# Kernel optimization log

Hardware: AMD Instinct MI355X
Metric: run time of the kernel (lower is better)

Reference implementation:

```python
import jax, jax.numpy as jnp
import numpy as np
from jax import lax
import math

C = 32            # num_channles
L_IN = 1024       # input signal length (forced by feature_size=520 constraint)
B = 1024          # batch


def _unfold(x, k, s):
    # x: (B, C, L) -> (B, C, n, k), torch Tensor.unfold(dim=2, size=k, step=s)
    n = (x.shape[-1] - k) // s + 1
    idx = np.arange(n)[:, None] * s + np.arange(k)[None, :]
    return x[..., idx]


def _always(x, w, b):
    # Conv1DAlwaysLayer: beta - sum_k (1 - window)*w, then relu, then leaky_relu(0.02)
    win = _unfold(x, 8, 2)                                  # (B,C,n,8)
    r = b[None, :, None] - jnp.einsum('bcnk,ck->bcn', 1.0 - win, w)
    return jax.nn.leaky_relu(jax.nn.relu(r), 0.02)


def _eventually(x, w, b):
    # Conv1DEventuallyLayer: relu(1 - (beta - sum_k window*w)), then leaky_relu(0.02)
    win = _unfold(x, 8, 2)
    r = 1.0 - (b[None, :, None] - jnp.einsum('bcnk,ck->bcn', win, w))
    return jax.nn.leaky_relu(jax.nn.relu(r), 0.02)


def _bn(x, g, b):
    # BatchNorm1d in training mode: batch statistics over (B, L), biased var
    m = x.mean(axis=(0, 2), keepdims=True)
    v = ((x - m) ** 2).mean(axis=(0, 2), keepdims=True)
    return (x - m) * jax.lax.rsqrt(v + 1e-5) * g[None, :, None] + b[None, :, None]


def _avgpool(x, k, s):
    return _unfold(x, k, s).mean(axis=-1)


def _maxpool(x, k, s):
    return _unfold(x, k, s).max(axis=-1)


def _laplace_filters(la_a, la_b):
    # LaplacePredicate filter bank: (C, 1, 16)
    A, ep, tal, f = 0.08, 0.03, 0.1, 50.0
    w = 2.0 * math.pi * f
    q = 1.0 - ep ** 2
    t = jnp.linspace(0.0, 1.0, 16, dtype=jnp.float32)       # kernel_size -> 16
    p = t[None, :] - (la_b / la_a)                           # (C,16)
    y = A * jnp.exp(-ep / math.sqrt(q) * (w * (p - tal))) * (-jnp.sin(w * (p - tal)))
    return y.reshape(C, 1, 16)


def setup_inputs() -> dict:
    key = jax.random.key(0)
    ks = jax.random.split(key, 32)
    rn = lambda k, shp: jax.random.normal(k, shp, dtype=jnp.float32)
    inp = {
        'x': rn(ks[0], (B, 1, L_IN)),
        # LaplacePredicate params
        'la_a': jnp.linspace(1.0, 10.0, C, dtype=jnp.float32).reshape(C, 1),
        'la_b': jnp.linspace(0.0, 10.0, C, dtype=jnp.float32).reshape(C, 1),
        'la_bias': rn(ks[1], (C,)),
        # BatchNorm after predicate
        'bn1_g': rn(ks[2], (C,)) * 0.1 + 1.0,
        'bn1_b': rn(ks[3], (C,)) * 0.1,
        # conv1d branch: Always -> Eventually -> MaxPool -> BN -> Eventually
        'a1_w': rn(ks[4], (C, 8)), 'a1_b': rn(ks[5], (C,)),
        'e1_w': rn(ks[6], (C, 8)), 'e1_b': rn(ks[7], (C,)),
        'bn2_g': rn(ks[8], (C,)) * 0.1 + 1.0, 'bn2_b': rn(ks[9], (C,)) * 0.1,
        'e2_w': rn(ks[10], (C, 8)), 'e2_b': rn(ks[11], (C,)),
        # conv1dFG branch: Eventually -> Always -> MaxPool -> BN -> Eventually
        'f1_w': rn(ks[12], (C, 8)), 'f1_b': rn(ks[13], (C,)),
        'fa_w': rn(ks[14], (C, 8)), 'fa_b': rn(ks[15], (C,)),
        'bn3_g': rn(ks[16], (C,)) * 0.1 + 1.0, 'bn3_b': rn(ks[17], (C,)) * 0.1,
        'f2_w': rn(ks[18], (C, 8)), 'f2_b': rn(ks[19], (C,)),
        # fc: 768 -> 1024 -> 512 -> 128 -> 10 (W stored (in,out))
        'w1': rn(ks[20], (768, 1024)) * (768 ** -0.5), 'b1': rn(ks[21], (1024,)) * 0.01,
        'w2': rn(ks[22], (1024, 512)) * (1024 ** -0.5), 'b2': rn(ks[23], (512,)) * 0.01,
        'w3': rn(ks[24], (512, 128)) * (512 ** -0.5), 'b3': rn(ks[25], (128,)) * 0.01,
        'w4': rn(ks[26], (128, 10)) * (128 ** -0.5), 'b4': rn(ks[27], (10,)) * 0.01,
    }
    return inp


def _forward(x, la_a, la_b, la_bias, bn1_g, bn1_b,
             a1_w, a1_b, e1_w, e1_b, bn2_g, bn2_b, e2_w, e2_b,
             f1_w, f1_b, fa_w, fa_b, bn3_g, bn3_b, f2_w, f2_b,
             w1, b1, w2, b2, w3, b3, w4, b4):
    # predicate_pos: LaplacePredicate -> BN -> AvgPool(3,2)
    filt = _laplace_filters(la_a, la_b)                      # (32,1,16)
    h = lax.conv_general_dilated(x, filt, window_strides=(1,),
                                 padding=[(16, 16)])         # (B,32,1041)
    h = h + la_bias[None, :, None]
    h = _bn(h, bn1_g, bn1_b)
    h = _avgpool(h, 3, 2)                                    # (B,32,520)
    # NOTE: fuseautoencoder/norm path in the source is dead code (result unused)
    # conv1d branch
    x1 = _always(h, a1_w, a1_b)                              # (B,32,257)
    x1 = _eventually(x1, e1_w, e1_b)                         # (B,32,125)
    x1 = _maxpool(x1, 4, 4)                                  # (B,32,31)
    x1 = _bn(x1, bn2_g, bn2_b)
    x1 = _eventually(x1, e2_w, e2_b)                         # (B,32,12)
    # conv1dFG branch
    x2 = _eventually(h, f1_w, f1_b)
    x2 = _always(x2, fa_w, fa_b)
    x2 = _maxpool(x2, 4, 4)
    x2 = _bn(x2, bn3_g, bn3_b)
    x2 = _eventually(x2, f2_w, f2_b)                         # (B,32,12)
    z = jnp.concatenate([x1, x2], axis=1).reshape(x.shape[0], -1)  # (B,768)
    z = jax.nn.relu(z @ w1 + b1)
    z = jax.nn.relu(z @ w2 + b2)    # Dropout -> identity (eval)
    z = jax.nn.relu(z @ w3 + b3)
    z = jax.nn.relu(z @ w4 + b4)
    return z                                                 # (B,10)


def reference(x, la_a, la_b, la_bias, bn1_g, bn1_b,
              a1_w, a1_b, e1_w, e1_b, bn2_g, bn2_b, e2_w, e2_b,
              f1_w, f1_b, fa_w, fa_b, bn3_g, bn3_b, f2_w, f2_b,
              w1, b1, w2, b2, w3, b3, w4, b4):
    return _forward(x, la_a, la_b, la_bias, bn1_g, bn1_b,
                    a1_w, a1_b, e1_w, e1_b, bn2_g, bn2_b, e2_w, e2_b,
                    f1_w, f1_b, fa_w, fa_b, bn3_g, bn3_b, f2_w, f2_b,
                    w1, b1, w2, b2, w3, b3, w4, b4)
```

## Files before the change

### kernel.cpp

```cpp
#include <hip/hip_runtime.h>
#include <math.h>


#define L_MP 31

using s8v = __attribute__((ext_vector_type(8))) short;
using f4v = __attribute__((ext_vector_type(4))) float;

__device__ __forceinline__ ushort f2bf(float f) {
    unsigned u = __float_as_uint(f);
    u += 0x7fffu + ((u >> 16) & 1u);
    return (ushort)(u >> 16);
}
__device__ __forceinline__ float bf2f(ushort u) {
    return __uint_as_float(((unsigned)u) << 16);
}

__global__ __launch_bounds__(256) void xstats_kernel(
    const float* __restrict__ x, double* __restrict__ xp)
{
    __shared__ __align__(16) float xr[1040];
    __shared__ float wred[4][17];
    int b = blockIdx.x, tid = threadIdx.x;
    for (int i = tid; i < 1024; i += 256) xr[i] = x[b * 1024 + i];
    if (tid < 16) xr[1024 + tid] = 0.f;
    __syncthreads();
    float acc[17];
#pragma unroll
    for (int d = 0; d < 17; ++d) acc[d] = 0.f;
    for (int p = tid; p < 1024; p += 256) {
        float v = xr[p];
        acc[16] += v;
#pragma unroll
        for (int d = 0; d < 16; ++d)
            acc[d] += v * xr[p + d];
    }
#pragma unroll
    for (int off = 32; off >= 1; off >>= 1)
#pragma unroll
        for (int d = 0; d < 17; ++d)
            acc[d] += __shfl_down(acc[d], off);
    int wave = tid >> 6, lane = tid & 63;
    if (lane == 0)
        for (int d = 0; d < 17; ++d) wred[wave][d] = acc[d];
    __syncthreads();
    if (tid < 17) {
        double tot = (double)wred[0][tid] + (double)wred[1][tid]
                   + (double)wred[2][tid] + (double)wred[3][tid];
        xp[tid * 1024 + b] = tot;
    }
}

__global__ __launch_bounds__(256) void reduce_x_kernel(
    const double* __restrict__ xp, double* __restrict__ stats)
{
    __shared__ double wr[4];
    int d = blockIdx.x, t = threadIdx.x;
    const double* r = xp + (size_t)d * 1024;
    double a = r[t] + r[t + 256] + r[t + 512] + r[t + 768];
#pragma unroll
    for (int off = 32; off >= 1; off >>= 1) a += __shfl_down(a, off);
    int wv = t >> 6, lane = t & 63;
    if (lane == 0) wr[wv] = a;
    __syncthreads();
    if (t == 0) stats[d] = wr[0] + wr[1] + wr[2] + wr[3];
}

__global__ __launch_bounds__(512) void prep_kernel(
    const double* __restrict__ stats,
    const float* __restrict__ la_a, const float* __restrict__ la_b,
    const float* __restrict__ bn1_g, const float* __restrict__ bn1_b,
    float* __restrict__ g18_out, float* __restrict__ a1d1_out)
{
    __shared__ float fs[32][16];
    int tid = threadIdx.x;
    if (tid < 512) {
        int c = tid >> 4, k = tid & 15;
        const double A = 0.08, ep = 0.03, tal = 0.1;
        const double w = 2.0 * 3.14159265358979323846 * 50.0;
        const double q = 1.0 - ep * ep;
        double t = (double)k / 15.0;
        double p = t - (double)la_b[c] / (double)la_a[c];
        double arg = w * (p - tal);
        double y = A * exp(-ep / sqrt(q) * arg) * (-sin(arg));
        fs[c][k] = (float)y;
    }
    __syncthreads();
    if (tid < 32) {
        int c = tid;
        for (int i = 0; i < 18; ++i) {
            float g = 0.f;
            for (int k = i - 2; k <= i; ++k)
                if (k >= 0 && k < 16) g += fs[c][k];
            g18_out[c * 18 + i] = g;
        }
        double Sf = 0.0;
        for (int k = 0; k < 16; ++k) Sf += (double)fs[c][k];
        double E2 = 0.0;
        for (int k = 0; k < 16; ++k)
            for (int k2 = 0; k2 < 16; ++k2)
                E2 += (double)fs[c][k] * (double)fs[c][k2]
                    * stats[k > k2 ? k - k2 : k2 - k];
        const double N = 1024.0 * 1041.0;
        double Sx = stats[16];
        double mc  = Sx * Sf / N;
        double var = E2 / N - mc * mc;
        double invstd = 1.0 / sqrt(var + 1e-5);
        float alpha = bn1_g[c] * (float)invstd;
        a1d1_out[c]      = alpha / 3.0f;
        a1d1_out[32 + c] = bn1_b[c] - (float)mc * alpha;
    }
}

__global__ __launch_bounds__(512) void branches_kernel(
    const float* __restrict__ x,
    const float* __restrict__ g18g, const float* __restrict__ a1d1,
    const float* __restrict__ a1w_g, const float* __restrict__ a1b_g,
    const float* __restrict__ e1w_g, const float* __restrict__ e1b_g,
    const float* __restrict__ f1w_g, const float* __restrict__ f1b_g,
    const float* __restrict__ faw_g, const float* __restrict__ fab_g,
    float* __restrict__ p1, float* __restrict__ p2,
    float* __restrict__ bp)
{
    __shared__ float xs[1140];
    __shared__ float g18s[32][18];
    __shared__ float wts[4][32][8];
    __shared__ float htail[32][6];

    int b = blockIdx.x, t = threadIdx.x;
    int wv = t >> 6, lane = t & 63;

    for (int i = t; i < 1072; i += 512) {
        float v = 0.f;
        if (i >= 16 && i < 1040) v = x[(size_t)b * 1024 + (i - 16)];
        xs[i + (i >> 4)] = v;
    }
    if (t < 288) ((float2*)&g18s[0][0])[t] = ((const float2*)g18g)[t];
    if (t < 256) {
        wts[0][0][t] = a1w_g[t];
        wts[1][0][t] = e1w_g[t];
        wts[2][0][t] = f1w_g[t];
        wts[3][0][t] = faw_g[t];
    }
    __syncthreads();

    if (t < 192) {
        int c = t / 6, e = t - 6 * (t / 6);
        float s = 0.f;
#pragma unroll
        for (int i = 0; i < 18; ++i) {
            int li = 1024 + 2 * e + i;
            s += g18s[c][i] * xs[li + (li >> 4)];
        }
        htail[c][e] = s * a1d1[c] + a1d1[32 + c];
    }
    __syncthreads();

    for (int cc = 0; cc < 4; ++cc) {
        int c = (cc << 3) + wv;
        float alpha = a1d1[c], delta = a1d1[32 + c];

        float hv[8];
        {
            float g[18];
#pragma unroll
            for (int i = 0; i < 18; ++i) g[i] = g18s[c][i];
            int base = 17 * lane;
            float xw[32];
#pragma unroll
            for (int q = 0; q < 16; ++q) xw[q] = xs[base + q];
#pragma unroll
            for (int q = 0; q < 16; ++q) xw[16 + q] = xs[base + 17 + q];
#pragma unroll
            for (int jj = 0; jj < 8; ++jj) {
                float s = 0.f;
#pragma unroll
                for (int i = 0; i < 18; ++i) s += g[i] * xw[2 * jj + i];
                hv[jj] = s * alpha + delta;
            }
        }

        float x1v[4], x2v[4];
        {
            float hx[14];
#pragma unroll
            for (int q = 0; q < 8; ++q) hx[q] = hv[q];
#pragma unroll
            for (int q = 0; q < 6; ++q) {
                float u = __shfl_down(hv[q], 1);
                float tl = htail[c][q];
                hx[8 + q] = (lane == 63) ? tl : u;
            }
            float wa[8], wf[8];
            float A1 = a1b_g[c], F1 = 1.f - f1b_g[c];
#pragma unroll
            for (int k = 0; k < 8; ++k) {
                wa[k] = wts[0][c][k];
                wf[k] = wts[2][c][k];
                A1 -= wa[k];
            }
#pragma unroll
            for (int nn = 0; nn < 4; ++nn) {
                float s1 = A1, s2 = F1;
#pragma unroll
                for (int k = 0; k < 8; ++k) {
                    float h = hx[2 * nn + k];
                    s1 += h * wa[k];
                    s2 += h * wf[k];
                }
                x1v[nn] = s1 > 0.f ? s1 : 0.f;
                x2v[nn] = s2 > 0.f ? s2 : 0.f;
            }
        }

        float y1v[2], y2v[2];
        {
            float xx1[10], xx2[10];
#pragma unroll
            for (int q = 0; q < 4; ++q) { xx1[q] = x1v[q]; xx2[q] = x2v[q]; }
#pragma unroll
            for (int q = 0; q < 4; ++q) {
                xx1[4 + q] = __shfl_down(x1v[q], 1);
                xx2[4 + q] = __shfl_down(x2v[q], 1);
            }
#pragma unroll
            for (int q = 0; q < 2; ++q) {
                xx1[8 + q] = __shfl_down(x1v[q], 2);
                xx2[8 + q] = __shfl_down(x2v[q], 2);
            }
            float we[8], wfa[8];
            float E1 = 1.f - e1b_g[c], FA = fab_g[c];
#pragma unroll
            for (int k = 0; k < 8; ++k) {
                we[k]  = wts[1][c][k];
                wfa[k] = wts[3][c][k];
                FA -= wfa[k];
            }
#pragma unroll
            for (int mm = 0; mm < 2; ++mm) {
                float s1 = E1, s2 = FA;
#pragma unroll
                for (int k = 0; k < 8; ++k) {
                    s1 += xx1[2 * mm + k] * we[k];
                    s2 += xx2[2 * mm + k] * wfa[k];
                }
                y1v[mm] = s1 > 0.f ? s1 : 0.f;
                y2v[mm] = s2 > 0.f ? s2 : 0.f;
            }
        }

        {
            int sa = 2 * lane, sb = 2 * lane + 1;
            float a0 = __shfl(y1v[0], sa), a1q = __shfl(y1v[1], sa);
            float a2 = __shfl(y1v[0], sb), a3 = __shfl(y1v[1], sb);
            float b0 = __shfl(y2v[0], sa), b1q = __shfl(y2v[1], sa);
            float b2 = __shfl(y2v[0], sb), b3 = __shfl(y2v[1], sb);
            float v1 = fmaxf(fmaxf(a0, a1q), fmaxf(a2, a3));
            float v2 = fmaxf(fmaxf(b0, b1q), fmaxf(b2, b3));
            bool valid = lane < L_MP;
            if (valid) {
                int bc = b * 32 + c;
                p1[(size_t)bc * L_MP + lane] = v1;
                p2[(size_t)bc * L_MP + lane] = v2;
            }
            float s1 = valid ? v1 : 0.f, q1 = valid ? v1 * v1 : 0.f;
            float s2 = valid ? v2 : 0.f, q2 = valid ? v2 * v2 : 0.f;
#pragma unroll
            for (int off = 16; off >= 1; off >>= 1) {
                s1 += __shfl_down(s1, off);
                q1 += __shfl_down(q1, off);
                s2 += __shfl_down(s2, off);
                q2 += __shfl_down(q2, off);
            }
            if (lane == 0) {
                bp[(size_t)(c)      * 1024 + b] = s1;
                bp[(size_t)(32 + c) * 1024 + b] = q1;
                bp[(size_t)(64 + c) * 1024 + b] = s2;
                bp[(size_t)(96 + c) * 1024 + b] = q2;
            }
        }
    }
}

__global__ __launch_bounds__(256) void reduce_bn_kernel(
    const float* __restrict__ bp, double* __restrict__ bn_d)
{
    __shared__ double wr[4];
    int r = blockIdx.x, t = threadIdx.x;
    const float* p = bp + (size_t)r * 1024;
    double a = (double)p[t] + (double)p[t + 256]
             + (double)p[t + 512] + (double)p[t + 768];
#pragma unroll
    for (int off = 32; off >= 1; off >>= 1) a += __shfl_down(a, off);
    int wv = t >> 6, lane = t & 63;
    if (lane == 0) wr[wv] = a;
    __syncthreads();
    if (t == 0) bn_d[r] = wr[0] + wr[1] + wr[2] + wr[3];
}

__global__ void bn23_finalize_kernel(
    const double* __restrict__ bn_d,
    const float* __restrict__ bn2_g, const float* __restrict__ bn2_b,
    const float* __restrict__ bn3_g, const float* __restrict__ bn3_b,
    float* __restrict__ ad23)
{
    int t = threadIdx.x;
    if (t < 64) {
        int br = t >> 5, c = t & 31;
        double sum = bn_d[br * 64 + c], sq = bn_d[br * 64 + 32 + c];
        const double N = 1024.0 * 31.0;
        double mean = sum / N;
        double var = sq / N - mean * mean;
        float g  = br ? bn3_g[c] : bn2_g[c];
        float be = br ? bn3_b[c] : bn2_b[c];
        float alpha = g * (float)(1.0 / sqrt(var + 1e-5));
        ad23[br * 64 + c]      = alpha;
        ad23[br * 64 + 32 + c] = be - (float)mean * alpha;
    }
}

__global__ __launch_bounds__(256) void final_ev_kernel(
    const float* __restrict__ p1, const float* __restrict__ p2,
    const float* __restrict__ e2w_g, const float* __restrict__ e2b_g,
    const float* __restrict__ f2w_g, const float* __restrict__ f2b_g,
    const float* __restrict__ ad23, ushort* __restrict__ z0)
{
    __shared__ float pr[2][32][31];
    __shared__ float w2s[2][32][8];
    __shared__ float al[2][32], de[2][32], eb[2][32];
    int b = blockIdx.x, tid = threadIdx.x;
    for (int i = tid; i < 992; i += 256) {
        pr[0][0][i] = p1[b * 992 + i];
        pr[1][0][i] = p2[b * 992 + i];
    }
    if (tid < 256) {
        w2s[0][0][tid] = e2w_g[tid];
        w2s[1][0][tid] = f2w_g[tid];
    }
    if (tid < 32) {
        al[0][tid] = ad23[tid];      de[0][tid] = ad23[32 + tid];
        al[1][tid] = ad23[64 + tid]; de[1][tid] = ad23[96 + tid];
        eb[0][tid] = e2b_g[tid];     eb[1][tid] = f2b_g[tid];
    }
    __syncthreads();
    for (int u = tid; u < 768; u += 256) {
        int br = u / 384, rem = u - br * 384;
        int c = rem / 12, tt = rem - c * 12;
        float a = al[br][c], d = de[br][c];
        float s = 1.f - eb[br][c];
#pragma unroll
        for (int k = 0; k < 8; ++k)
            s += (pr[br][c][2 * tt + k] * a + d) * w2s[br][c][k];
        z0[(size_t)b * 768 + u] = f2bf(s > 0.f ? s : 0.f);
    }
}

__global__ __launch_bounds__(256) void transpose_bf16_kernel(
    const float* __restrict__ W, ushort* __restrict__ Wt, int K, int N)
{
    __shared__ float tile[32][33];
    int n0 = blockIdx.x * 32, k0 = blockIdx.y * 32;
    int tx = threadIdx.x & 31, ty = threadIdx.x >> 5;
#pragma unroll
    for (int i = 0; i < 4; ++i)
        tile[ty + 8 * i][tx] = W[(size_t)(k0 + ty + 8 * i) * N + n0 + tx];
    __syncthreads();
#pragma unroll
    for (int i = 0; i < 4; ++i)
        Wt[(size_t)(n0 + ty + 8 * i) * K + k0 + tx] = f2bf(tile[tx][ty + 8 * i]);
}

__global__ __launch_bounds__(256) void gemm_mfma_kernel(
    const ushort* __restrict__ A, const ushort* __restrict__ Bt,
    const float* __restrict__ bias, ushort* __restrict__ C,
    int N, int K)
{
    int w = blockIdx.x * 4 + (threadIdx.x >> 6);
    int lane = threadIdx.x & 63;
    int ntiles = N >> 4;
    int mt = w / ntiles, nt = w - mt * ntiles;
    int r = lane & 15, q = lane >> 4;
    const ushort* ap = A + (size_t)(mt * 16 + r) * K + q * 8;
    const ushort* bp = Bt + (size_t)(nt * 16 + r) * K + q * 8;
    f4v acc = {0.f, 0.f, 0.f, 0.f};
    int nk = K >> 5;
    s8v a0 = *(const s8v*)ap;
    s8v b0 = *(const s8v*)bp;
#pragma unroll 4
    for (int i = 0; i < nk; ++i) {
        int j = (i + 1 < nk) ? i + 1 : i;
        s8v a1 = *(const s8v*)(ap + (size_t)j * 32);
        s8v b1 = *(const s8v*)(bp + (size_t)j * 32);
        acc = __builtin_amdgcn_mfma_f32_16x16x32_bf16(a0, b0, acc, 0, 0, 0);
        a0 = a1; b0 = b1;
    }
    float bv = bias[nt * 16 + r];
    int row0 = mt * 16 + q * 4;
    int col = nt * 16 + r;
#pragma unroll
    for (int rr = 0; rr < 4; ++rr) {
        float v = acc[rr] + bv;
        v = v > 0.f ? v : 0.f;
        C[(size_t)(row0 + rr) * N + col] = f2bf(v);
    }
}

__global__ __launch_bounds__(256) void fc4_kernel(
    const ushort* __restrict__ z3, const float* __restrict__ w4,
    const float* __restrict__ b4, float* __restrict__ out)
{
    int g = blockIdx.x * 256 + threadIdx.x;
    if (g >= 1024 * 10) return;
    int m = g / 10, n = g - m * 10;
    float acc = b4[n];
#pragma unroll 8
    for (int k = 0; k < 128; ++k)
        acc += bf2f(z3[m * 128 + k]) * w4[k * 10 + n];
    out[g] = acc > 0.f ? acc : 0.f;
}

extern "C" void kernel_launch(void* const* d_in, const int* in_sizes, int n_in,
                              void* d_out, int out_size, void* d_ws, size_t ws_size,
                              hipStream_t stream)
{
    (void)in_sizes; (void)n_in; (void)out_size; (void)ws_size;
    const float* x      = (const float*)d_in[0];
    const float* la_a   = (const float*)d_in[1];
    const float* la_b   = (const float*)d_in[2];
    const float* bn1_g  = (const float*)d_in[4];
    const float* bn1_b  = (const float*)d_in[5];
    const float* a1_w   = (const float*)d_in[6];
    const float* a1_b   = (const float*)d_in[7];
    const float* e1_w   = (const float*)d_in[8];
    const float* e1_b   = (const float*)d_in[9];
    const float* bn2_g  = (const float*)d_in[10];
    const float* bn2_b  = (const float*)d_in[11];
    const float* e2_w   = (const float*)d_in[12];
    const float* e2_b   = (const float*)d_in[13];
    const float* f1_w   = (const float*)d_in[14];
    const float* f1_b   = (const float*)d_in[15];
    const float* fa_w   = (const float*)d_in[16];
    const float* fa_b   = (const float*)d_in[17];
    const float* bn3_g  = (const float*)d_in[18];
    const float* bn3_b  = (const float*)d_in[19];
    const float* f2_w   = (const float*)d_in[20];
    const float* f2_b   = (const float*)d_in[21];
    const float* w1     = (const float*)d_in[22];
    const float* b1     = (const float*)d_in[23];
    const float* w2     = (const float*)d_in[24];
    const float* b2     = (const float*)d_in[25];
    const float* w3     = (const float*)d_in[26];
    const float* b3     = (const float*)d_in[27];
    const float* w4     = (const float*)d_in[28];
    const float* b4     = (const float*)d_in[29];
    float* out = (float*)d_out;

    char* w = (char*)d_ws;
    double* stats_d = (double*)(w + 0);
    double* bn_d    = (double*)(w + 256);
    float* g18      = (float*)(w + 1536);
    float* a1d1     = (float*)(w + 3840);
    float* ad23     = (float*)(w + 4096);
    float* p1       = (float*)(w + 8192);
    float* p2       = (float*)(w + 4071424);
    ushort* z0bf    = (ushort*)(w + 8134656);
    ushort* z1bf    = (ushort*)(w + 9707520);
    ushort* z2bf    = (ushort*)(w + 11804672);
    ushort* z3bf    = (ushort*)(w + 12853248);
    ushort* wt1     = (ushort*)(w + 13115392);
    ushort* wt2     = (ushort*)(w + 14688256);
    ushort* wt3     = (ushort*)(w + 15736832);
    double* xp      = (double*)(w + 15867904);
    float*  bpart   = (float*)(w + 16007168);

    transpose_bf16_kernel<<<dim3(32, 24), 256, 0, stream>>>(w1, wt1, 768, 1024);
    transpose_bf16_kernel<<<dim3(16, 32), 256, 0, stream>>>(w2, wt2, 1024, 512);
    transpose_bf16_kernel<<<dim3(4, 16), 256, 0, stream>>>(w3, wt3, 512, 128);

    xstats_kernel<<<1024, 256, 0, stream>>>(x, xp);
    reduce_x_kernel<<<17, 256, 0, stream>>>(xp, stats_d);
    prep_kernel<<<1, 512, 0, stream>>>(stats_d, la_a, la_b, bn1_g, bn1_b, g18, a1d1);
    branches_kernel<<<1024, 512, 0, stream>>>(
        x, g18, a1d1, a1_w, a1_b, e1_w, e1_b, f1_w, f1_b, fa_w, fa_b,
        p1, p2, bpart);
    reduce_bn_kernel<<<128, 256, 0, stream>>>(bpart, bn_d);
    bn23_finalize_kernel<<<1, 64, 0, stream>>>(bn_d, bn2_g, bn2_b, bn3_g, bn3_b, ad23);
    final_ev_kernel<<<1024, 256, 0, stream>>>(p1, p2, e2_w, e2_b, f2_w, f2_b, ad23, z0bf);

    gemm_mfma_kernel<<<1024, 256, 0, stream>>>(z0bf, wt1, b1, z1bf, 1024, 768);
    gemm_mfma_kernel<<<512, 256, 0, stream>>>(z1bf, wt2, b2, z2bf, 512, 1024);
    gemm_mfma_kernel<<<128, 256, 0, stream>>>(z2bf, wt3, b3, z3bf, 128, 512);
    fc4_kernel<<<40, 256, 0, stream>>>(z3bf, w4, b4, out);
}
```

Before: 234.6 us.

## Merge small reduction kernels, split branches per channel half, batch weight transposes

```diff
diff --git a/kernel.cpp b/kernel.cpp
--- a/kernel.cpp
+++ b/kernel.cpp
@@ -51,30 +51,26 @@
     }
 }
 
-__global__ __launch_bounds__(256) void reduce_x_kernel(
-    const double* __restrict__ xp, double* __restrict__ stats)
-{
-    __shared__ double wr[4];
-    int d = blockIdx.x, t = threadIdx.x;
-    const double* r = xp + (size_t)d * 1024;
-    double a = r[t] + r[t + 256] + r[t + 512] + r[t + 768];
-#pragma unroll
-    for (int off = 32; off >= 1; off >>= 1) a += __shfl_down(a, off);
-    int wv = t >> 6, lane = t & 63;
-    if (lane == 0) wr[wv] = a;
-    __syncthreads();
-    if (t == 0) stats[d] = wr[0] + wr[1] + wr[2] + wr[3];
-}
-
 __global__ __launch_bounds__(512) void prep_kernel(
-    const double* __restrict__ stats,
+    const double* __restrict__ xp,
     const float* __restrict__ la_a, const float* __restrict__ la_b,
     const float* __restrict__ bn1_g, const float* __restrict__ bn1_b,
     float* __restrict__ g18_out, float* __restrict__ a1d1_out)
 {
+    __shared__ double stats[17];
     __shared__ float fs[32][16];
-    int tid = threadIdx.x;
-    if (tid < 512) {
+    int tid = threadIdx.x, wv = tid >> 6, lane = tid & 63;
+
+    for (int row = wv; row < 17; row += 8) {
+        const double* r = xp + (size_t)row * 1024;
+        double a = 0.0;
+        for (int i = lane; i < 1024; i += 64) a += r[i];
+#pragma unroll
+        for (int off = 32; off >= 1; off >>= 1) a += __shfl_down(a, off);
+        if (lane == 0) stats[row] = a;
+    }
+
+    {
         int c = tid >> 4, k = tid & 15;
         const double A = 0.08, ep = 0.03, tal = 0.1;
         const double w = 2.0 * 3.14159265358979323846 * 50.0;
@@ -112,65 +108,71 @@
     }
 }
 
-__global__ __launch_bounds__(512) void branches_kernel(
+__global__ __launch_bounds__(256) void branches_kernel(
     const float* __restrict__ x,
     const float* __restrict__ g18g, const float* __restrict__ a1d1,
     const float* __restrict__ a1w_g, const float* __restrict__ a1b_g,
     const float* __restrict__ e1w_g, const float* __restrict__ e1b_g,
     const float* __restrict__ f1w_g, const float* __restrict__ f1b_g,
     const float* __restrict__ faw_g, const float* __restrict__ fab_g,
-    float* __restrict__ p1, float* __restrict__ p2,
-    float* __restrict__ bp)
+    float* __restrict__ p1, float* __restrict__ p2)
 {
     __shared__ float xs[1140];
-    __shared__ float g18s[32][18];
-    __shared__ float wts[4][32][8];
-    __shared__ float htail[32][6];
-
-    int b = blockIdx.x, t = threadIdx.x;
+    __shared__ float g18s[16][18];
+    __shared__ float wts[4][16][8];
+    __shared__ float htail[16][6];
+
+    int blk = blockIdx.x;
+    int b = blk >> 1, hf = blk & 1;
+    int t = threadIdx.x;
     int wv = t >> 6, lane = t & 63;
 
-    for (int i = t; i < 1072; i += 512) {
+    for (int i = t; i < 1072; i += 256) {
         float v = 0.f;
         if (i >= 16 && i < 1040) v = x[(size_t)b * 1024 + (i - 16)];
         xs[i + (i >> 4)] = v;
     }
-    if (t < 288) ((float2*)&g18s[0][0])[t] = ((const float2*)g18g)[t];
-    if (t < 256) {
-        wts[0][0][t] = a1w_g[t];
-        wts[1][0][t] = e1w_g[t];
-        wts[2][0][t] = f1w_g[t];
-        wts[3][0][t] = faw_g[t];
-    }
-    __syncthreads();
-
-    if (t < 192) {
-        int c = t / 6, e = t - 6 * (t / 6);
+    if (t < 144) ((float2*)&g18s[0][0])[t] = ((const float2*)(g18g + hf * 288))[t];
+    if (t < 128) {
+        wts[0][0][t] = a1w_g[hf * 128 + t];
+        wts[1][0][t] = e1w_g[hf * 128 + t];
+        wts[2][0][t] = f1w_g[hf * 128 + t];
+        wts[3][0][t] = faw_g[hf * 128 + t];
+    }
+    __syncthreads();
+
+    if (t < 96) {
+        int cl = t / 6, e = t - 6 * (t / 6);
+        int cg = hf * 16 + cl;
         float s = 0.f;
 #pragma unroll
         for (int i = 0; i < 18; ++i) {
             int li = 1024 + 2 * e + i;
-            s += g18s[c][i] * xs[li + (li >> 4)];
-        }
-        htail[c][e] = s * a1d1[c] + a1d1[32 + c];
-    }
-    __syncthreads();
+            s += g18s[cl][i] * xs[li + (li >> 4)];
+        }
+        htail[cl][e] = s * a1d1[cg] + a1d1[32 + cg];
+    }
+    __syncthreads();
+
+    float xw[32];
+    {
+        int base = 17 * lane;
+#pragma unroll
+        for (int q = 0; q < 16; ++q) xw[q] = xs[base + q];
+#pragma unroll
+        for (int q = 0; q < 16; ++q) xw[16 + q] = xs[base + 17 + q];
+    }
 
     for (int cc = 0; cc < 4; ++cc) {
-        int c = (cc << 3) + wv;
-        float alpha = a1d1[c], delta = a1d1[32 + c];
+        int cl = wv * 4 + cc;
+        int cg = hf * 16 + cl;
+        float alpha = a1d1[cg], delta = a1d1[32 + cg];
 
         float hv[8];
         {
             float g[18];
 #pragma unroll
-            for (int i = 0; i < 18; ++i) g[i] = g18s[c][i];
-            int base = 17 * lane;
-            float xw[32];
-#pragma unroll
-            for (int q = 0; q < 16; ++q) xw[q] = xs[base + q];
-#pragma unroll
-            for (int q = 0; q < 16; ++q) xw[16 + q] = xs[base + 17 + q];
+            for (int i = 0; i < 18; ++i) g[i] = g18s[cl][i];
 #pragma unroll
             for (int jj = 0; jj < 8; ++jj) {
                 float s = 0.f;
@@ -188,15 +190,15 @@
 #pragma unroll
             for (int q = 0; q < 6; ++q) {
                 float u = __shfl_down(hv[q], 1);
-                float tl = htail[c][q];
+                float tl = htail[cl][q];
                 hx[8 + q] = (lane == 63) ? tl : u;
             }
             float wa[8], wf[8];
-            float A1 = a1b_g[c], F1 = 1.f - f1b_g[c];
+            float A1 = a1b_g[cg], F1 = 1.f - f1b_g[cg];
 #pragma unroll
             for (int k = 0; k < 8; ++k) {
-                wa[k] = wts[0][c][k];
-                wf[k] = wts[2][c][k];
+                wa[k] = wts[0][cl][k];
+                wf[k] = wts[2][cl][k];
                 A1 -= wa[k];
             }
 #pragma unroll
@@ -229,11 +231,11 @@
                 xx2[8 + q] = __shfl_down(x2v[q], 2);
             }
             float we[8], wfa[8];
-            float E1 = 1.f - e1b_g[c], FA = fab_g[c];
+            float E1 = 1.f - e1b_g[cg], FA = fab_g[cg];
 #pragma unroll
             for (int k = 0; k < 8; ++k) {
-                we[k]  = wts[1][c][k];
-                wfa[k] = wts[3][c][k];
+                we[k]  = wts[1][cl][k];
+                wfa[k] = wts[3][cl][k];
                 FA -= wfa[k];
             }
 #pragma unroll
@@ -250,63 +252,73 @@
         }
 
         {
-            int sa = 2 * lane, sb = 2 * lane + 1;
-            float a0 = __shfl(y1v[0], sa), a1q = __shfl(y1v[1], sa);
-            float a2 = __shfl(y1v[0], sb), a3 = __shfl(y1v[1], sb);
-            float b0 = __shfl(y2v[0], sa), b1q = __shfl(y2v[1], sa);
-            float b2 = __shfl(y2v[0], sb), b3 = __shfl(y2v[1], sb);
-            float v1 = fmaxf(fmaxf(a0, a1q), fmaxf(a2, a3));
-            float v2 = fmaxf(fmaxf(b0, b1q), fmaxf(b2, b3));
-            bool valid = lane < L_MP;
-            if (valid) {
-                int bc = b * 32 + c;
-                p1[(size_t)bc * L_MP + lane] = v1;
-                p2[(size_t)bc * L_MP + lane] = v2;
-            }
-            float s1 = valid ? v1 : 0.f, q1 = valid ? v1 * v1 : 0.f;
-            float s2 = valid ? v2 : 0.f, q2 = valid ? v2 * v2 : 0.f;
-#pragma unroll
-            for (int off = 16; off >= 1; off >>= 1) {
-                s1 += __shfl_down(s1, off);
-                q1 += __shfl_down(q1, off);
-                s2 += __shfl_down(s2, off);
-                q2 += __shfl_down(q2, off);
-            }
-            if (lane == 0) {
-                bp[(size_t)(c)      * 1024 + b] = s1;
-                bp[(size_t)(32 + c) * 1024 + b] = q1;
-                bp[(size_t)(64 + c) * 1024 + b] = s2;
-                bp[(size_t)(96 + c) * 1024 + b] = q2;
-            }
-        }
-    }
-}
-
-__global__ __launch_bounds__(256) void reduce_bn_kernel(
-    const float* __restrict__ bp, double* __restrict__ bn_d)
-{
-    __shared__ double wr[4];
-    int r = blockIdx.x, t = threadIdx.x;
-    const float* p = bp + (size_t)r * 1024;
-    double a = (double)p[t] + (double)p[t + 256]
-             + (double)p[t + 512] + (double)p[t + 768];
-#pragma unroll
-    for (int off = 32; off >= 1; off >>= 1) a += __shfl_down(a, off);
-    int wv = t >> 6, lane = t & 63;
-    if (lane == 0) wr[wv] = a;
-    __syncthreads();
-    if (t == 0) bn_d[r] = wr[0] + wr[1] + wr[2] + wr[3];
-}
-
-__global__ void bn23_finalize_kernel(
+            float m1 = fmaxf(y1v[0], y1v[1]);
+            float m2 = fmaxf(y2v[0], y2v[1]);
+            float n1 = __shfl_down(m1, 1);
+            float n2 = __shfl_down(m2, 1);
+            int tt = lane >> 1;
+            if (!(lane & 1) && tt < L_MP) {
+                int bc = b * 32 + cg;
+                p1[(size_t)bc * L_MP + tt] = fmaxf(m1, n1);
+                p2[(size_t)bc * L_MP + tt] = fmaxf(m2, n2);
+            }
+        }
+    }
+}
+
+__global__ __launch_bounds__(256) void pstats_kernel(
+    const float* __restrict__ p1, const float* __restrict__ p2,
+    double* __restrict__ bn_d)
+{
+    __shared__ double wr[4][2];
+    int bx = blockIdx.x, arr = bx >> 5, c = bx & 31;
+    const float* p = arr ? p2 : p1;
+    int t = threadIdx.x, wv = t >> 6, lane = t & 63;
+    double s = 0.0, q = 0.0;
+    for (int bb = t; bb < 1024; bb += 256) {
+        const float* r = p + ((size_t)bb * 32 + c) * L_MP;
+#pragma unroll
+        for (int j = 0; j < L_MP; ++j) {
+            double v = (double)r[j];
+            s += v; q += v * v;
+        }
+    }
+#pragma unroll
+    for (int off = 32; off >= 1; off >>= 1) {
+        s += __shfl_down(s, off);
+        q += __shfl_down(q, off);
+    }
+    if (lane == 0) { wr[wv][0] = s; wr[wv][1] = q; }
+    __syncthreads();
+    if (t == 0) {
+        bn_d[arr * 64 + c]      = wr[0][0] + wr[1][0] + wr[2][0] + wr[3][0];
+        bn_d[arr * 64 + 32 + c] = wr[0][1] + wr[1][1] + wr[2][1] + wr[3][1];
+    }
+}
+
+__global__ __launch_bounds__(256) void final_ev_kernel(
+    const float* __restrict__ p1, const float* __restrict__ p2,
+    const float* __restrict__ e2w_g, const float* __restrict__ e2b_g,
+    const float* __restrict__ f2w_g, const float* __restrict__ f2b_g,
     const double* __restrict__ bn_d,
     const float* __restrict__ bn2_g, const float* __restrict__ bn2_b,
     const float* __restrict__ bn3_g, const float* __restrict__ bn3_b,
-    float* __restrict__ ad23)
-{
-    int t = threadIdx.x;
-    if (t < 64) {
-        int br = t >> 5, c = t & 31;
+    ushort* __restrict__ z0)
+{
+    __shared__ float pr[2][32][31];
+    __shared__ float w2s[2][32][8];
+    __shared__ float al[2][32], de[2][32], eb[2][32];
+    int b = blockIdx.x, tid = threadIdx.x;
+    for (int i = tid; i < 992; i += 256) {
+        pr[0][0][i] = p1[b * 992 + i];
+        pr[1][0][i] = p2[b * 992 + i];
+    }
+    {
+        w2s[0][0][tid] = e2w_g[tid];
+        w2s[1][0][tid] = f2w_g[tid];
+    }
+    if (tid < 64) {
+        int br = tid >> 5, c = tid & 31;
         double sum = bn_d[br * 64 + c], sq = bn_d[br * 64 + 32 + c];
         const double N = 1024.0 * 31.0;
         double mean = sum / N;
@@ -314,33 +326,9 @@
         float g  = br ? bn3_g[c] : bn2_g[c];
         float be = br ? bn3_b[c] : bn2_b[c];
         float alpha = g * (float)(1.0 / sqrt(var + 1e-5));
-        ad23[br * 64 + c]      = alpha;
-        ad23[br * 64 + 32 + c] = be - (float)mean * alpha;
-    }
-}
-
-__global__ __launch_bounds__(256) void final_ev_kernel(
-    const float* __restrict__ p1, const float* __restrict__ p2,
-    const float* __restrict__ e2w_g, const float* __restrict__ e2b_g,
-    const float* __restrict__ f2w_g, const float* __restrict__ f2b_g,
-    const float* __restrict__ ad23, ushort* __restrict__ z0)
-{
-    __shared__ float pr[2][32][31];
-    __shared__ float w2s[2][32][8];
-    __shared__ float al[2][32], de[2][32], eb[2][32];
-    int b = blockIdx.x, tid = threadIdx.x;
-    for (int i = tid; i < 992; i += 256) {
-        pr[0][0][i] = p1[b * 992 + i];
-        pr[1][0][i] = p2[b * 992 + i];
-    }
-    if (tid < 256) {
-        w2s[0][0][tid] = e2w_g[tid];
-        w2s[1][0][tid] = f2w_g[tid];
-    }
-    if (tid < 32) {
-        al[0][tid] = ad23[tid];      de[0][tid] = ad23[32 + tid];
-        al[1][tid] = ad23[64 + tid]; de[1][tid] = ad23[96 + tid];
-        eb[0][tid] = e2b_g[tid];     eb[1][tid] = f2b_g[tid];
+        al[br][c] = alpha;
+        de[br][c] = be - (float)mean * alpha;
+        eb[br][c] = br ? f2b_g[c] : e2b_g[c];
     }
     __syncthreads();
     for (int u = tid; u < 768; u += 256) {
@@ -355,11 +343,18 @@
     }
 }
 
-__global__ __launch_bounds__(256) void transpose_bf16_kernel(
-    const float* __restrict__ W, ushort* __restrict__ Wt, int K, int N)
+__global__ __launch_bounds__(256) void transpose_all_kernel(
+    const float* __restrict__ w1, const float* __restrict__ w2,
+    const float* __restrict__ w3,
+    ushort* __restrict__ wt1, ushort* __restrict__ wt2, ushort* __restrict__ wt3)
 {
     __shared__ float tile[32][33];
-    int n0 = blockIdx.x * 32, k0 = blockIdx.y * 32;
+    int bx = blockIdx.x;
+    const float* W; ushort* Wt; int K, N, ntx, tl;
+    if (bx < 768)       { W = w1; Wt = wt1; K = 768;  N = 1024; ntx = 32; tl = bx; }
+    else if (bx < 1280) { W = w2; Wt = wt2; K = 1024; N = 512;  ntx = 16; tl = bx - 768; }
+    else                { W = w3; Wt = wt3; K = 512;  N = 128;  ntx = 4;  tl = bx - 1280; }
+    int n0 = (tl % ntx) * 32, k0 = (tl / ntx) * 32;
     int tx = threadIdx.x & 31, ty = threadIdx.x >> 5;
 #pragma unroll
     for (int i = 0; i < 4; ++i)
@@ -456,11 +451,9 @@
     float* out = (float*)d_out;
 
     char* w = (char*)d_ws;
-    double* stats_d = (double*)(w + 0);
     double* bn_d    = (double*)(w + 256);
     float* g18      = (float*)(w + 1536);
     float* a1d1     = (float*)(w + 3840);
-    float* ad23     = (float*)(w + 4096);
     float* p1       = (float*)(w + 8192);
     float* p2       = (float*)(w + 4071424);
     ushort* z0bf    = (ushort*)(w + 8134656);
@@ -471,22 +464,15 @@
     ushort* wt2     = (ushort*)(w + 14688256);
     ushort* wt3     = (ushort*)(w + 15736832);
     double* xp      = (double*)(w + 15867904);
-    float*  bpart   = (float*)(w + 16007168);
-
-    transpose_bf16_kernel<<<dim3(32, 24), 256, 0, stream>>>(w1, wt1, 768, 1024);
-    transpose_bf16_kernel<<<dim3(16, 32), 256, 0, stream>>>(w2, wt2, 1024, 512);
-    transpose_bf16_kernel<<<dim3(4, 16), 256, 0, stream>>>(w3, wt3, 512, 128);
 
     xstats_kernel<<<1024, 256, 0, stream>>>(x, xp);
-    reduce_x_kernel<<<17, 256, 0, stream>>>(xp, stats_d);
-    prep_kernel<<<1, 512, 0, stream>>>(stats_d, la_a, la_b, bn1_g, bn1_b, g18, a1d1);
-    branches_kernel<<<1024, 512, 0, stream>>>(
-        x, g18, a1d1, a1_w, a1_b, e1_w, e1_b, f1_w, f1_b, fa_w, fa_b,
-        p1, p2, bpart);
-    reduce_bn_kernel<<<128, 256, 0, stream>>>(bpart, bn_d);
-    bn23_finalize_kernel<<<1, 64, 0, stream>>>(bn_d, bn2_g, bn2_b, bn3_g, bn3_b, ad23);
-    final_ev_kernel<<<1024, 256, 0, stream>>>(p1, p2, e2_w, e2_b, f2_w, f2_b, ad23, z0bf);
-
+    prep_kernel<<<1, 512, 0, stream>>>(xp, la_a, la_b, bn1_g, bn1_b, g18, a1d1);
+    branches_kernel<<<2048, 256, 0, stream>>>(
+        x, g18, a1d1, a1_w, a1_b, e1_w, e1_b, f1_w, f1_b, fa_w, fa_b, p1, p2);
+    pstats_kernel<<<64, 256, 0, stream>>>(p1, p2, bn_d);
+    final_ev_kernel<<<1024, 256, 0, stream>>>(
+        p1, p2, e2_w, e2_b, f2_w, f2_b, bn_d, bn2_g, bn2_b, bn3_g, bn3_b, z0bf);
+    transpose_all_kernel<<<1344, 256, 0, stream>>>(w1, w2, w3, wt1, wt2, wt3);
     gemm_mfma_kernel<<<1024, 256, 0, stream>>>(z0bf, wt1, b1, z1bf, 1024, 768);
     gemm_mfma_kernel<<<512, 256, 0, stream>>>(z1bf, wt2, b2, z2bf, 512, 1024);
     gemm_mfma_kernel<<<128, 256, 0, stream>>>(z2bf, wt3, b3, z3bf, 128, 512);
```

Measured after the change: 237.0 us. No clear change (+1.0%).
